# Optimization experiments

Hardware: AMD Instinct MI355X
Metric: run time of the kernel (lower is better)

The kernel has to match this reference:

```python
import jax, jax.numpy as jnp
import numpy as np

B, N, C = 16, 1024, 768
E, H, D, K = 8, 192, 4, 2


def setup_inputs() -> dict:
    key = jax.random.key(0)
    ks = jax.random.split(key, 8)
    std = 0.02
    return {
        "x": jax.random.normal(ks[0], (B, N, C), jnp.float32),
        "task_ids": jax.random.randint(ks[1], (B,), 0, D),
        "eps": jax.random.normal(ks[2], (B, N, E), jnp.float32),
        "gate_w": jax.random.normal(ks[3], (D, C, 2 * E), jnp.float32) * std,
        "fc1_w": jax.random.normal(ks[4], (E, H, C), jnp.float32) * std,
        "fc1_b": jnp.zeros((E, H), jnp.float32),
        "fc2_w": jax.random.normal(ks[5], (E, C, H), jnp.float32) * std,
        "fc2_b": jnp.zeros((E, C), jnp.float32),
    }


def reference(x, task_ids, eps, gate_w, fc1_w, fc1_b, fc2_w, fc2_b):
    # per-sample gate selected by domain/task id: [B,N,2E]
    total_w = jnp.einsum("bnc,bce->bne", x, gate_w[task_ids])
    clean_logits, raw_noise = jnp.split(total_w, 2, axis=-1)  # [B,N,E] each
    noise_stddev = jax.nn.softplus(raw_noise) + 0.01
    logits = clean_logits + eps * noise_stddev  # [B,N,E]
    exp_wise_sum = logits.sum(axis=1)  # [B,E]

    top_k_logits, top_k_idx = jax.lax.top_k(exp_wise_sum, K)  # [B,K]
    m1 = top_k_logits.min(axis=1, keepdims=True)
    m2 = top_k_logits.max(axis=1, keepdims=True)
    scaled = (top_k_logits - m1) / (m2 - m1 + 1e-6)
    top_k_gates = jax.nn.softmax(scaled, axis=1)  # [B,K]

    gates_full = jnp.zeros((B, E), x.dtype).at[
        jnp.arange(B)[:, None], top_k_idx
    ].set(top_k_gates)  # [B,E]

    # dense all-expert adapter compute (faithful to original torch.stack)
    h = jnp.einsum("bnc,ehc->benh", x, fc1_w) + fc1_b[None, :, None, :]
    h = jax.nn.gelu(h, approximate=False)
    expert_outs = jnp.einsum("benh,ech->benc", h, fc2_w) + fc2_b[None, :, None, :]

    tot_x = jnp.einsum("be,benc->bnc", gates_full, expert_outs)
    return x + tot_x
```

## Files before the change

kernel.cpp:

```cpp
#include <hip/hip_runtime.h>

#define B_ 16
#define N_ 1024
#define C_ 768
#define E_ 8
#define H_ 192

typedef __bf16 bf16x8 __attribute__((ext_vector_type(8)));
typedef float  f32x4  __attribute__((ext_vector_type(4)));

__global__ __launch_bounds__(256) void prep_kernel(
    const float* __restrict__ w1, const float* __restrict__ w2,
    const float* __restrict__ gw,
    __bf16* __restrict__ pw1, __bf16* __restrict__ pw2,
    float* __restrict__ gwT) {
  int idx = blockIdx.x * 256 + threadIdx.x;
  const int nW4 = (E_ * H_ * C_) / 4;
  if (idx >= nW4) return;
  int flat = idx * 4;
  int e = flat / (H_ * C_);
  int r = flat - e * (H_ * C_);

  {
    float4 a = *(const float4*)(w1 + (size_t)flat);
    int n = r / C_;
    int c = r - n * C_;
    size_t o = ((size_t)(e * 24 + (c >> 5)) * 192 + n) * 32 + (c & 31);
    pw1[o + 0] = (__bf16)a.x; pw1[o + 1] = (__bf16)a.y;
    pw1[o + 2] = (__bf16)a.z; pw1[o + 3] = (__bf16)a.w;
  }
  {
    float4 a = *(const float4*)(w2 + (size_t)flat);
    int n = r / H_;
    int h = r - n * H_;
    size_t o = ((size_t)(e * 6 + (h >> 5)) * 768 + n) * 32 + (h & 31);
    pw2[o + 0] = (__bf16)a.x; pw2[o + 1] = (__bf16)a.y;
    pw2[o + 2] = (__bf16)a.z; pw2[o + 3] = (__bf16)a.w;
  }
  if (idx < (4 * 16 * C_) / 4) {
    int f = idx * 4;
    int d = f / (16 * C_);
    int rr = f - d * (16 * C_);
    int j = rr / C_;
    int c = rr - j * C_;
    const float* src = gw + (size_t)d * C_ * 16 + j;
    float4 v;
    v.x = src[(size_t)(c + 0) * 16]; v.y = src[(size_t)(c + 1) * 16];
    v.z = src[(size_t)(c + 2) * 16]; v.w = src[(size_t)(c + 3) * 16];
    *(float4*)(gwT + (size_t)f) = v;
  }
}

__global__ __launch_bounds__(256, 3) void gate_kernel(
    const float* __restrict__ x, const int* __restrict__ task_ids,
    const float* __restrict__ eps, const float* __restrict__ gwT,
    float* __restrict__ psums) {
  const int b = blockIdx.x >> 6;
  const int token0 = (blockIdx.x & 63) * 16;
  const int tid = threadIdx.x;

  __shared__ __align__(16) float xt[16][772];
  __shared__ float sc[16][16];
  __shared__ float red[16][8];

  const float* xbase = x + ((size_t)b * N_ + token0) * C_;
  for (int it = 0; it < 12; ++it) {
    int chunk = it * 256 + tid;
    int row = chunk / 192;
    int col4 = chunk - row * 192;
    float4 v = *(const float4*)(xbase + (size_t)row * C_ + col4 * 4);
    *(float4*)&xt[row][col4 * 4] = v;
  }
  __syncthreads();

  const int t = tid & 15;
  const int j = tid >> 4;
  const int task = task_ids[b];
  const float* wrow = gwT + ((size_t)task * 16 + j) * C_;
  float acc = 0.0f;
#pragma unroll 4
  for (int c = 0; c < C_; c += 4) {
    float4 xv = *(const float4*)&xt[t][c];
    float4 wv = *(const float4*)(wrow + c);
    acc += xv.x * wv.x + xv.y * wv.y + xv.z * wv.z + xv.w * wv.w;
  }
  sc[t][j] = acc;
  __syncthreads();
  if (j < 8) {
    float clean = sc[t][j];
    float raw = sc[t][j + 8];
    float sp = (raw > 20.0f) ? raw : log1pf(expf(raw));
    red[t][j] = clean +
        eps[((size_t)b * N_ + token0 + t) * E_ + j] * (sp + 0.01f);
  }
  __syncthreads();
  if (tid < 8) {
    float s = 0.0f;
#pragma unroll
    for (int tt = 0; tt < 16; ++tt) s += red[tt][tid];
    psums[(size_t)blockIdx.x * 8 + tid] = s;
  }
}

#define SMEM_EXPERT (64 * 776 * 2 + 64 * 200 * 2 + 32)

__global__ __launch_bounds__(512, 2) void expert_kernel(
    const float* __restrict__ x, const __bf16* __restrict__ pw1,
    const __bf16* __restrict__ pw2, const float* __restrict__ fc1_b,
    const float* __restrict__ fc2_b, const float* __restrict__ psums,
    float* __restrict__ out) {
  const int bid = blockIdx.x;
  const int sxc = bid >> 3;
  const int b = (bid & 7) * 2 + (sxc >> 4);
  const int token0 = (sxc & 15) * 64;
  const int tid = threadIdx.x;
  const int wave = tid >> 6;
  const int wm = wave >> 2;
  const int wn = wave & 3;
  const int lane = tid & 63;
  const int ln = lane & 15;
  const int q8 = (lane >> 4) * 8;
  const int q4 = (lane >> 4) * 4;
  const int arow = wm * 32;

  extern __shared__ char smem[];
  __bf16 (*xs)[776] = reinterpret_cast<__bf16(*)[776]>(smem);
  __bf16 (*hs)[200] = reinterpret_cast<__bf16(*)[200]>(smem + 99328);
  float* smc = reinterpret_cast<float*>(smem + 99328 + 25600);

  {
    float v = psums[(((size_t)b << 6) | lane) * 8 + wave];
#pragma unroll
    for (int off = 32; off; off >>= 1) v += __shfl_down(v, off);
    if (lane == 0) smc[wave] = v;
  }
  __syncthreads();

  int e_idx[2]; float gate_v[2];
  {
    float best = -INFINITY, best2 = -INFINITY;
    int i1 = 0, i2 = 0;
#pragma unroll
    for (int e = 0; e < E_; ++e) {
      float v = smc[e];
      if (v > best) { best2 = best; i2 = i1; best = v; i1 = e; }
      else if (v > best2) { best2 = v; i2 = e; }
    }
    float d = best - best2;
    float st = d / (d + 1e-6f);
    float et = expf(st);
    e_idx[0] = i1; gate_v[0] = et / (et + 1.0f);
    e_idx[1] = i2; gate_v[1] = 1.0f / (et + 1.0f);
  }

  bf16x8 bq[4][3];
  {
    const __bf16* w1l = pw1 + (size_t)e_idx[0] * (24 * 192 * 32)
                            + (size_t)(wn * 48 + ln) * 32 + q8;
#pragma unroll
    for (int k0 = 0; k0 < 4; ++k0)
#pragma unroll
      for (int jj = 0; jj < 3; ++jj)
        bq[k0][jj] = *(const bf16x8*)(w1l + (size_t)k0 * 6144 + jj * 512);
  }

  const float* xbase = x + ((size_t)b * N_ + token0) * C_;
  for (int it = 0; it < 12; ++it) {
    int chunk = it * 512 + tid;
    int row = chunk / 96;
    int col8 = chunk - row * 96;
    const float* p = xbase + (size_t)row * C_ + col8 * 8;
    float4 v0 = *(const float4*)p;
    float4 v1 = *(const float4*)(p + 4);
    bf16x8 tv;
    tv[0] = (__bf16)v0.x; tv[1] = (__bf16)v0.y; tv[2] = (__bf16)v0.z; tv[3] = (__bf16)v0.w;
    tv[4] = (__bf16)v1.x; tv[5] = (__bf16)v1.y; tv[6] = (__bf16)v1.z; tv[7] = (__bf16)v1.w;
    *(bf16x8*)&xs[row][col8 * 8] = tv;
  }
  __syncthreads();

  f32x4 c2[2][12] = {};

  for (int kx = 0; kx < 2; ++kx) {
    const int e = e_idx[kx];
    const float g = gate_v[kx];

    const __bf16* w1l = pw1 + (size_t)e * (24 * 192 * 32)
                            + (size_t)(wn * 48 + ln) * 32 + q8;
    if (kx == 1) {
#pragma unroll
      for (int k0 = 0; k0 < 4; ++k0)
#pragma unroll
        for (int jj = 0; jj < 3; ++jj)
          bq[k0][jj] = *(const bf16x8*)(w1l + (size_t)k0 * 6144 + jj * 512);
    }
    bf16x8 aq[4][2];
#pragma unroll
    for (int k0 = 0; k0 < 4; ++k0) {
      aq[k0][0] = *(const bf16x8*)&xs[arow + ln][k0 * 32 + q8];
      aq[k0][1] = *(const bf16x8*)&xs[arow + 16 + ln][k0 * 32 + q8];
    }
    f32x4 c1[2][3] = {};
#pragma unroll
    for (int kb = 0; kb < 24; ++kb) {
      const int p = kb & 3;
#pragma unroll
      for (int jj = 0; jj < 3; ++jj) {
        c1[0][jj] = __builtin_amdgcn_mfma_f32_16x16x32_bf16(aq[p][0], bq[p][jj], c1[0][jj], 0, 0, 0);
        c1[1][jj] = __builtin_amdgcn_mfma_f32_16x16x32_bf16(aq[p][1], bq[p][jj], c1[1][jj], 0, 0, 0);
      }
      if (kb < 20) {
        const int kn = kb + 4;
        const __bf16* nx = w1l + (size_t)kn * 6144;
#pragma unroll
        for (int jj = 0; jj < 3; ++jj) bq[p][jj] = *(const bf16x8*)(nx + jj * 512);
        aq[p][0] = *(const bf16x8*)&xs[arow + ln][kn * 32 + q8];
        aq[p][1] = *(const bf16x8*)&xs[arow + 16 + ln][kn * 32 + q8];
      }
    }
#pragma unroll
    for (int jj = 0; jj < 3; ++jj) {
      int col = wn * 48 + jj * 16 + ln;
      float b1 = fc1_b[e * H_ + col];
#pragma unroll
      for (int m = 0; m < 2; ++m) {
#pragma unroll
        for (int r = 0; r < 4; ++r) {
          int row = arow + m * 16 + q4 + r;
          float v = c1[m][jj][r] + b1;
          float gl = 0.5f * v * (1.0f + erff(v * 0.70710678118f));
          hs[row][col] = (__bf16)(g * gl);
        }
      }
    }
    __syncthreads();

    const __bf16* w2l = pw2 + (size_t)e * (6 * 768 * 32)
                            + (size_t)(wn * 192 + ln) * 32 + q8;
    bf16x8 bh[3][6], av[3][2];
#pragma unroll
    for (int s0 = 0; s0 < 3; ++s0) {
      const __bf16* src = w2l + (size_t)(s0 >> 1) * 24576;
#pragma unroll
      for (int jj = 0; jj < 6; ++jj)
        bh[s0][jj] = *(const bf16x8*)(src + ((s0 & 1) * 6 + jj) * 512);
    }
    av[0][0] = *(const bf16x8*)&hs[arow + ln][q8];
    av[0][1] = *(const bf16x8*)&hs[arow + 16 + ln][q8];
    av[1][0] = *(const bf16x8*)&hs[arow + ln][32 + q8];
    av[1][1] = *(const bf16x8*)&hs[arow + 16 + ln][32 + q8];
#pragma unroll
    for (int st = 0; st < 12; ++st) {
      const int kb = st >> 1;
      const int half = st & 1;
      const int p = st % 3;
      const int as = kb % 3;
#pragma unroll
      for (int jj = 0; jj < 6; ++jj) {
        const int cj = half * 6 + jj;
        c2[0][cj] = __builtin_amdgcn_mfma_f32_16x16x32_bf16(av[as][0], bh[p][jj], c2[0][cj], 0, 0, 0);
        c2[1][cj] = __builtin_amdgcn_mfma_f32_16x16x32_bf16(av[as][1], bh[p][jj], c2[1][cj], 0, 0, 0);
      }
      if (st < 9) {
        const int s2 = st + 3;
        const int kb2 = s2 >> 1, half2 = s2 & 1;
        const __bf16* src = w2l + (size_t)kb2 * 24576;
#pragma unroll
        for (int jj = 0; jj < 6; ++jj)
          bh[p][jj] = *(const bf16x8*)(src + (half2 * 6 + jj) * 512);
        if (half2 == 0) {
          av[kb2 % 3][0] = *(const bf16x8*)&hs[arow + ln][kb2 * 32 + q8];
          av[kb2 % 3][1] = *(const bf16x8*)&hs[arow + 16 + ln][kb2 * 32 + q8];
        }
      }
    }
    __syncthreads();
  }

  const float* xr = x + ((size_t)b * N_ + token0) * C_;
  float* outr = out + ((size_t)b * N_ + token0) * C_;
#pragma unroll
  for (int jj = 0; jj < 12; ++jj) {
    int col = wn * 192 + jj * 16 + ln;
    float b2t = gate_v[0] * fc2_b[e_idx[0] * C_ + col] +
                gate_v[1] * fc2_b[e_idx[1] * C_ + col];
#pragma unroll
    for (int m = 0; m < 2; ++m) {
#pragma unroll
      for (int r = 0; r < 4; ++r) {
        int row = arow + m * 16 + q4 + r;
        size_t off = (size_t)row * C_ + col;
        outr[off] = xr[off] + c2[m][jj][r] + b2t;
      }
    }
  }
}

extern "C" void kernel_launch(void* const* d_in, const int* in_sizes, int n_in,
                              void* d_out, int out_size, void* d_ws, size_t ws_size,
                              hipStream_t stream) {
  const float* x      = (const float*)d_in[0];
  const int*   task   = (const int*)d_in[1];
  const float* eps    = (const float*)d_in[2];
  const float* gate_w = (const float*)d_in[3];
  const float* fc1_w  = (const float*)d_in[4];
  const float* fc1_b  = (const float*)d_in[5];
  const float* fc2_w  = (const float*)d_in[6];
  const float* fc2_b  = (const float*)d_in[7];
  float* out = (float*)d_out;

  const size_t nW = (size_t)E_ * H_ * C_;
  __bf16* pw1 = (__bf16*)d_ws;
  __bf16* pw2 = pw1 + nW;
  float* gwT   = (float*)((char*)d_ws + 2 * nW * sizeof(__bf16));
  float* psums = gwT + 4 * 16 * C_;

  prep_kernel<<<(nW / 4 + 255) / 256, 256, 0, stream>>>(fc1_w, fc2_w, gate_w,
                                                        pw1, pw2, gwT);
  gate_kernel<<<B_ * 64, 256, 0, stream>>>(x, task, eps, gwT, psums);

  hipFuncSetAttribute(reinterpret_cast<const void*>(expert_kernel),
                      hipFuncAttributeMaxDynamicSharedMemorySize, SMEM_EXPERT);
  expert_kernel<<<B_ * 16, 512, SMEM_EXPERT, stream>>>(
      x, pw1, pw2, fc1_b, fc2_b, psums, out);
}
```

Baseline: 206.0 us.

## Double expert kernel block to 1024 threads, one 16-row tile per wave

The expert kernel moves from 512 to 1024 threads per block, so each wave computes a 16-row M tile instead of 32 rows. The weight and activation prefetch pipelines become shallower (3-stage for fc1, double-buffered for fc2), which cuts per-thread registers to allow more waves. The trade-off is that each B-fragment weight load from global memory now feeds only one MFMA row tile, so weight traffic per FLOP doubles. With launch_bounds(1024,4), register pressure may also force spills.

Result: slower. 228.0 us (+10.7%).

```diff
diff --git a/kernel.cpp b/kernel.cpp
--- a/kernel.cpp
+++ b/kernel.cpp
@@ -104,7 +104,7 @@
 
 #define SMEM_EXPERT (64 * 776 * 2 + 64 * 200 * 2 + 32)
 
-__global__ __launch_bounds__(512, 2) void expert_kernel(
+__global__ __launch_bounds__(1024, 4) void expert_kernel(
     const float* __restrict__ x, const __bf16* __restrict__ pw1,
     const __bf16* __restrict__ pw2, const float* __restrict__ fc1_b,
     const float* __restrict__ fc2_b, const float* __restrict__ psums,
@@ -121,14 +121,14 @@
   const int ln = lane & 15;
   const int q8 = (lane >> 4) * 8;
   const int q4 = (lane >> 4) * 4;
-  const int arow = wm * 32;
+  const int arow = wm * 16;
 
   extern __shared__ char smem[];
   __bf16 (*xs)[776] = reinterpret_cast<__bf16(*)[776]>(smem);
   __bf16 (*hs)[200] = reinterpret_cast<__bf16(*)[200]>(smem + 99328);
   float* smc = reinterpret_cast<float*>(smem + 99328 + 25600);
 
-  {
+  if (wave < 8) {
     float v = psums[(((size_t)b << 6) | lane) * 8 + wave];
 #pragma unroll
     for (int off = 32; off; off >>= 1) v += __shfl_down(v, off);
@@ -153,20 +153,20 @@
     e_idx[1] = i2; gate_v[1] = 1.0f / (et + 1.0f);
   }
 
-  bf16x8 bq[4][3];
+  bf16x8 bq[3][3];
   {
     const __bf16* w1l = pw1 + (size_t)e_idx[0] * (24 * 192 * 32)
                             + (size_t)(wn * 48 + ln) * 32 + q8;
 #pragma unroll
-    for (int k0 = 0; k0 < 4; ++k0)
+    for (int k0 = 0; k0 < 3; ++k0)
 #pragma unroll
       for (int jj = 0; jj < 3; ++jj)
         bq[k0][jj] = *(const bf16x8*)(w1l + (size_t)k0 * 6144 + jj * 512);
   }
 
   const float* xbase = x + ((size_t)b * N_ + token0) * C_;
-  for (int it = 0; it < 12; ++it) {
-    int chunk = it * 512 + tid;
+  for (int it = 0; it < 6; ++it) {
+    int chunk = it * 1024 + tid;
     int row = chunk / 96;
     int col8 = chunk - row * 96;
     const float* p = xbase + (size_t)row * C_ + col8 * 8;
@@ -179,7 +179,7 @@
   }
   __syncthreads();
 
-  f32x4 c2[2][12] = {};
+  f32x4 c2[12] = {};
 
   for (int kx = 0; kx < 2; ++kx) {
     const int e = e_idx[kx];
@@ -189,33 +189,28 @@
                             + (size_t)(wn * 48 + ln) * 32 + q8;
     if (kx == 1) {
 #pragma unroll
-      for (int k0 = 0; k0 < 4; ++k0)
+      for (int k0 = 0; k0 < 3; ++k0)
 #pragma unroll
         for (int jj = 0; jj < 3; ++jj)
           bq[k0][jj] = *(const bf16x8*)(w1l + (size_t)k0 * 6144 + jj * 512);
     }
-    bf16x8 aq[4][2];
-#pragma unroll
-    for (int k0 = 0; k0 < 4; ++k0) {
-      aq[k0][0] = *(const bf16x8*)&xs[arow + ln][k0 * 32 + q8];
-      aq[k0][1] = *(const bf16x8*)&xs[arow + 16 + ln][k0 * 32 + q8];
-    }
-    f32x4 c1[2][3] = {};
+    bf16x8 aq[3];
+#pragma unroll
+    for (int k0 = 0; k0 < 3; ++k0)
+      aq[k0] = *(const bf16x8*)&xs[arow + ln][k0 * 32 + q8];
+    f32x4 c1[3] = {};
 #pragma unroll
     for (int kb = 0; kb < 24; ++kb) {
-      const int p = kb & 3;
-#pragma unroll
-      for (int jj = 0; jj < 3; ++jj) {
-        c1[0][jj] = __builtin_amdgcn_mfma_f32_16x16x32_bf16(aq[p][0], bq[p][jj], c1[0][jj], 0, 0, 0);
-        c1[1][jj] = __builtin_amdgcn_mfma_f32_16x16x32_bf16(aq[p][1], bq[p][jj], c1[1][jj], 0, 0, 0);
-      }
-      if (kb < 20) {
-        const int kn = kb + 4;
+      const int p = kb % 3;
+#pragma unroll
+      for (int jj = 0; jj < 3; ++jj)
+        c1[jj] = __builtin_amdgcn_mfma_f32_16x16x32_bf16(aq[p], bq[p][jj], c1[jj], 0, 0, 0);
+      if (kb < 21) {
+        const int kn = kb + 3;
         const __bf16* nx = w1l + (size_t)kn * 6144;
 #pragma unroll
         for (int jj = 0; jj < 3; ++jj) bq[p][jj] = *(const bf16x8*)(nx + jj * 512);
-        aq[p][0] = *(const bf16x8*)&xs[arow + ln][kn * 32 + q8];
-        aq[p][1] = *(const bf16x8*)&xs[arow + 16 + ln][kn * 32 + q8];
+        aq[p] = *(const bf16x8*)&xs[arow + ln][kn * 32 + q8];
       }
     }
 #pragma unroll
@@ -223,55 +218,40 @@
       int col = wn * 48 + jj * 16 + ln;
       float b1 = fc1_b[e * H_ + col];
 #pragma unroll
-      for (int m = 0; m < 2; ++m) {
-#pragma unroll
-        for (int r = 0; r < 4; ++r) {
-          int row = arow + m * 16 + q4 + r;
-          float v = c1[m][jj][r] + b1;
-          float gl = 0.5f * v * (1.0f + erff(v * 0.70710678118f));
-          hs[row][col] = (__bf16)(g * gl);
-        }
+      for (int r = 0; r < 4; ++r) {
+        int row = arow + q4 + r;
+        float v = c1[jj][r] + b1;
+        float gl = 0.5f * v * (1.0f + erff(v * 0.70710678118f));
+        hs[row][col] = (__bf16)(g * gl);
       }
     }
     __syncthreads();
 
     const __bf16* w2l = pw2 + (size_t)e * (6 * 768 * 32)
                             + (size_t)(wn * 192 + ln) * 32 + q8;
-    bf16x8 bh[3][6], av[3][2];
-#pragma unroll
-    for (int s0 = 0; s0 < 3; ++s0) {
-      const __bf16* src = w2l + (size_t)(s0 >> 1) * 24576;
-#pragma unroll
-      for (int jj = 0; jj < 6; ++jj)
-        bh[s0][jj] = *(const bf16x8*)(src + ((s0 & 1) * 6 + jj) * 512);
-    }
-    av[0][0] = *(const bf16x8*)&hs[arow + ln][q8];
-    av[0][1] = *(const bf16x8*)&hs[arow + 16 + ln][q8];
-    av[1][0] = *(const bf16x8*)&hs[arow + ln][32 + q8];
-    av[1][1] = *(const bf16x8*)&hs[arow + 16 + ln][32 + q8];
+    bf16x8 bh[2][6], av[2];
+#pragma unroll
+    for (int jj = 0; jj < 6; ++jj) bh[0][jj] = *(const bf16x8*)(w2l + jj * 512);
+    av[0] = *(const bf16x8*)&hs[arow + ln][q8];
 #pragma unroll
     for (int st = 0; st < 12; ++st) {
       const int kb = st >> 1;
       const int half = st & 1;
-      const int p = st % 3;
-      const int as = kb % 3;
+      const int p = st & 1;
+      if (st < 11) {
+        const int s2 = st + 1;
+        const int kb2 = s2 >> 1, half2 = s2 & 1;
+        const __bf16* src = w2l + (size_t)kb2 * 24576;
+#pragma unroll
+        for (int jj = 0; jj < 6; ++jj)
+          bh[p ^ 1][jj] = *(const bf16x8*)(src + (half2 * 6 + jj) * 512);
+        if (half2 == 0)
+          av[kb2 & 1] = *(const bf16x8*)&hs[arow + ln][kb2 * 32 + q8];
+      }
 #pragma unroll
       for (int jj = 0; jj < 6; ++jj) {
         const int cj = half * 6 + jj;
-        c2[0][cj] = __builtin_amdgcn_mfma_f32_16x16x32_bf16(av[as][0], bh[p][jj], c2[0][cj], 0, 0, 0);
-        c2[1][cj] = __builtin_amdgcn_mfma_f32_16x16x32_bf16(av[as][1], bh[p][jj], c2[1][cj], 0, 0, 0);
-      }
-      if (st < 9) {
-        const int s2 = st + 3;
-        const int kb2 = s2 >> 1, half2 = s2 & 1;
-        const __bf16* src = w2l + (size_t)kb2 * 24576;
-#pragma unroll
-        for (int jj = 0; jj < 6; ++jj)
-          bh[p][jj] = *(const bf16x8*)(src + (half2 * 6 + jj) * 512);
-        if (half2 == 0) {
-          av[kb2 % 3][0] = *(const bf16x8*)&hs[arow + ln][kb2 * 32 + q8];
-          av[kb2 % 3][1] = *(const bf16x8*)&hs[arow + 16 + ln][kb2 * 32 + q8];
-        }
+        c2[cj] = __builtin_amdgcn_mfma_f32_16x16x32_bf16(av[kb & 1], bh[p][jj], c2[cj], 0, 0, 0);
       }
     }
     __syncthreads();
@@ -285,13 +265,10 @@
     float b2t = gate_v[0] * fc2_b[e_idx[0] * C_ + col] +
                 gate_v[1] * fc2_b[e_idx[1] * C_ + col];
 #pragma unroll
-    for (int m = 0; m < 2; ++m) {
-#pragma unroll
-      for (int r = 0; r < 4; ++r) {
-        int row = arow + m * 16 + q4 + r;
-        size_t off = (size_t)row * C_ + col;
-        outr[off] = xr[off] + c2[m][jj][r] + b2t;
-      }
+    for (int r = 0; r < 4; ++r) {
+      int row = arow + q4 + r;
+      size_t off = (size_t)row * C_ + col;
+      outr[off] = xr[off] + c2[jj][r] + b2t;
     }
   }
 }
@@ -321,6 +298,6 @@
 
   hipFuncSetAttribute(reinterpret_cast<const void*>(expert_kernel),
                       hipFuncAttributeMaxDynamicSharedMemorySize, SMEM_EXPERT);
-  expert_kernel<<<B_ * 16, 512, SMEM_EXPERT, stream>>>(
+  expert_kernel<<<B_ * 16, 1024, SMEM_EXPERT, stream>>>(
       x, pw1, pw2, fc1_b, fc2_b, psums, out);
 }
```

## Use 12 waves per block with 6-way column split in expert kernel

Applied to the files above, without the earlier changes.

Raises the expert kernel block from 512 to 768 threads, so 12 waves are arranged as 2x6 instead of 2x4. Each wave now covers 32 hidden columns in the first GEMM and 128 output columns in the second. The second GEMM is restructured into two passes with double-buffered weight prefetch, which cuts per-wave register pressure and exposes more waves for latency hiding. The grid stays at 256 blocks, so each block gets more parallelism but loses some per-wave prefetch depth. Launch bounds become (768,3), which tightens the register cap and could cause spills.

Result: no change. 205.6 us (-0.2%).

```diff
diff --git a/kernel.cpp b/kernel.cpp
--- a/kernel.cpp
+++ b/kernel.cpp
@@ -104,7 +104,7 @@
 
 #define SMEM_EXPERT (64 * 776 * 2 + 64 * 200 * 2 + 32)
 
-__global__ __launch_bounds__(512, 2) void expert_kernel(
+__global__ __launch_bounds__(768, 3) void expert_kernel(
     const float* __restrict__ x, const __bf16* __restrict__ pw1,
     const __bf16* __restrict__ pw2, const float* __restrict__ fc1_b,
     const float* __restrict__ fc2_b, const float* __restrict__ psums,
@@ -115,8 +115,8 @@
   const int token0 = (sxc & 15) * 64;
   const int tid = threadIdx.x;
   const int wave = tid >> 6;
-  const int wm = wave >> 2;
-  const int wn = wave & 3;
+  const int wm = wave / 6;
+  const int wn = wave - wm * 6;
   const int lane = tid & 63;
   const int ln = lane & 15;
   const int q8 = (lane >> 4) * 8;
@@ -128,7 +128,7 @@
   __bf16 (*hs)[200] = reinterpret_cast<__bf16(*)[200]>(smem + 99328);
   float* smc = reinterpret_cast<float*>(smem + 99328 + 25600);
 
-  {
+  if (wave < 8) {
     float v = psums[(((size_t)b << 6) | lane) * 8 + wave];
 #pragma unroll
     for (int off = 32; off; off >>= 1) v += __shfl_down(v, off);
@@ -153,20 +153,20 @@
     e_idx[1] = i2; gate_v[1] = 1.0f / (et + 1.0f);
   }
 
-  bf16x8 bq[4][3];
+  bf16x8 bq[3][2];
   {
     const __bf16* w1l = pw1 + (size_t)e_idx[0] * (24 * 192 * 32)
-                            + (size_t)(wn * 48 + ln) * 32 + q8;
-#pragma unroll
-    for (int k0 = 0; k0 < 4; ++k0)
-#pragma unroll
-      for (int jj = 0; jj < 3; ++jj)
+                            + (size_t)(wn * 32 + ln) * 32 + q8;
+#pragma unroll
+    for (int k0 = 0; k0 < 3; ++k0)
+#pragma unroll
+      for (int jj = 0; jj < 2; ++jj)
         bq[k0][jj] = *(const bf16x8*)(w1l + (size_t)k0 * 6144 + jj * 512);
   }
 
   const float* xbase = x + ((size_t)b * N_ + token0) * C_;
-  for (int it = 0; it < 12; ++it) {
-    int chunk = it * 512 + tid;
+  for (int it = 0; it < 8; ++it) {
+    int chunk = it * 768 + tid;
     int row = chunk / 96;
     int col8 = chunk - row * 96;
     const float* p = xbase + (size_t)row * C_ + col8 * 8;
@@ -179,48 +179,48 @@
   }
   __syncthreads();
 
-  f32x4 c2[2][12] = {};
+  f32x4 c2[2][8] = {};
 
   for (int kx = 0; kx < 2; ++kx) {
     const int e = e_idx[kx];
     const float g = gate_v[kx];
 
     const __bf16* w1l = pw1 + (size_t)e * (24 * 192 * 32)
-                            + (size_t)(wn * 48 + ln) * 32 + q8;
+                            + (size_t)(wn * 32 + ln) * 32 + q8;
     if (kx == 1) {
 #pragma unroll
-      for (int k0 = 0; k0 < 4; ++k0)
-#pragma unroll
-        for (int jj = 0; jj < 3; ++jj)
+      for (int k0 = 0; k0 < 3; ++k0)
+#pragma unroll
+        for (int jj = 0; jj < 2; ++jj)
           bq[k0][jj] = *(const bf16x8*)(w1l + (size_t)k0 * 6144 + jj * 512);
     }
-    bf16x8 aq[4][2];
-#pragma unroll
-    for (int k0 = 0; k0 < 4; ++k0) {
+    bf16x8 aq[3][2];
+#pragma unroll
+    for (int k0 = 0; k0 < 3; ++k0) {
       aq[k0][0] = *(const bf16x8*)&xs[arow + ln][k0 * 32 + q8];
       aq[k0][1] = *(const bf16x8*)&xs[arow + 16 + ln][k0 * 32 + q8];
     }
-    f32x4 c1[2][3] = {};
+    f32x4 c1[2][2] = {};
 #pragma unroll
     for (int kb = 0; kb < 24; ++kb) {
-      const int p = kb & 3;
-#pragma unroll
-      for (int jj = 0; jj < 3; ++jj) {
+      const int p = kb % 3;
+#pragma unroll
+      for (int jj = 0; jj < 2; ++jj) {
         c1[0][jj] = __builtin_amdgcn_mfma_f32_16x16x32_bf16(aq[p][0], bq[p][jj], c1[0][jj], 0, 0, 0);
         c1[1][jj] = __builtin_amdgcn_mfma_f32_16x16x32_bf16(aq[p][1], bq[p][jj], c1[1][jj], 0, 0, 0);
       }
-      if (kb < 20) {
-        const int kn = kb + 4;
+      if (kb < 21) {
+        const int kn = kb + 3;
         const __bf16* nx = w1l + (size_t)kn * 6144;
 #pragma unroll
-        for (int jj = 0; jj < 3; ++jj) bq[p][jj] = *(const bf16x8*)(nx + jj * 512);
+        for (int jj = 0; jj < 2; ++jj) bq[p][jj] = *(const bf16x8*)(nx + jj * 512);
         aq[p][0] = *(const bf16x8*)&xs[arow + ln][kn * 32 + q8];
         aq[p][1] = *(const bf16x8*)&xs[arow + 16 + ln][kn * 32 + q8];
       }
     }
 #pragma unroll
-    for (int jj = 0; jj < 3; ++jj) {
-      int col = wn * 48 + jj * 16 + ln;
+    for (int jj = 0; jj < 2; ++jj) {
+      int col = wn * 32 + jj * 16 + ln;
       float b1 = fc1_b[e * H_ + col];
 #pragma unroll
       for (int m = 0; m < 2; ++m) {
@@ -235,42 +235,31 @@
     }
     __syncthreads();
 
-    const __bf16* w2l = pw2 + (size_t)e * (6 * 768 * 32)
-                            + (size_t)(wn * 192 + ln) * 32 + q8;
-    bf16x8 bh[3][6], av[3][2];
-#pragma unroll
-    for (int s0 = 0; s0 < 3; ++s0) {
-      const __bf16* src = w2l + (size_t)(s0 >> 1) * 24576;
-#pragma unroll
-      for (int jj = 0; jj < 6; ++jj)
-        bh[s0][jj] = *(const bf16x8*)(src + ((s0 & 1) * 6 + jj) * 512);
-    }
-    av[0][0] = *(const bf16x8*)&hs[arow + ln][q8];
-    av[0][1] = *(const bf16x8*)&hs[arow + 16 + ln][q8];
-    av[1][0] = *(const bf16x8*)&hs[arow + ln][32 + q8];
-    av[1][1] = *(const bf16x8*)&hs[arow + 16 + ln][32 + q8];
-#pragma unroll
-    for (int st = 0; st < 12; ++st) {
-      const int kb = st >> 1;
-      const int half = st & 1;
-      const int p = st % 3;
-      const int as = kb % 3;
-#pragma unroll
-      for (int jj = 0; jj < 6; ++jj) {
-        const int cj = half * 6 + jj;
-        c2[0][cj] = __builtin_amdgcn_mfma_f32_16x16x32_bf16(av[as][0], bh[p][jj], c2[0][cj], 0, 0, 0);
-        c2[1][cj] = __builtin_amdgcn_mfma_f32_16x16x32_bf16(av[as][1], bh[p][jj], c2[1][cj], 0, 0, 0);
-      }
-      if (st < 9) {
-        const int s2 = st + 3;
-        const int kb2 = s2 >> 1, half2 = s2 & 1;
-        const __bf16* src = w2l + (size_t)kb2 * 24576;
-#pragma unroll
-        for (int jj = 0; jj < 6; ++jj)
-          bh[p][jj] = *(const bf16x8*)(src + (half2 * 6 + jj) * 512);
-        if (half2 == 0) {
-          av[kb2 % 3][0] = *(const bf16x8*)&hs[arow + ln][kb2 * 32 + q8];
-          av[kb2 % 3][1] = *(const bf16x8*)&hs[arow + 16 + ln][kb2 * 32 + q8];
+#pragma unroll
+    for (int pass = 0; pass < 2; ++pass) {
+      const __bf16* w2l = pw2 + (size_t)e * (6 * 768 * 32)
+                              + (size_t)(wn * 128 + pass * 64 + ln) * 32 + q8;
+      bf16x8 bh[2][4], av[2][2];
+#pragma unroll
+      for (int jj = 0; jj < 4; ++jj) bh[0][jj] = *(const bf16x8*)(w2l + jj * 512);
+      av[0][0] = *(const bf16x8*)&hs[arow + ln][q8];
+      av[0][1] = *(const bf16x8*)&hs[arow + 16 + ln][q8];
+#pragma unroll
+      for (int kb = 0; kb < 6; ++kb) {
+        const int p = kb & 1;
+        if (kb < 5) {
+          const __bf16* src = w2l + (size_t)(kb + 1) * 24576;
+#pragma unroll
+          for (int jj = 0; jj < 4; ++jj)
+            bh[p ^ 1][jj] = *(const bf16x8*)(src + jj * 512);
+          av[p ^ 1][0] = *(const bf16x8*)&hs[arow + ln][(kb + 1) * 32 + q8];
+          av[p ^ 1][1] = *(const bf16x8*)&hs[arow + 16 + ln][(kb + 1) * 32 + q8];
+        }
+#pragma unroll
+        for (int jj = 0; jj < 4; ++jj) {
+          const int cj = pass * 4 + jj;
+          c2[0][cj] = __builtin_amdgcn_mfma_f32_16x16x32_bf16(av[p][0], bh[p][jj], c2[0][cj], 0, 0, 0);
+          c2[1][cj] = __builtin_amdgcn_mfma_f32_16x16x32_bf16(av[p][1], bh[p][jj], c2[1][cj], 0, 0, 0);
         }
       }
     }
@@ -280,8 +269,8 @@
   const float* xr = x + ((size_t)b * N_ + token0) * C_;
   float* outr = out + ((size_t)b * N_ + token0) * C_;
 #pragma unroll
-  for (int jj = 0; jj < 12; ++jj) {
-    int col = wn * 192 + jj * 16 + ln;
+  for (int jj = 0; jj < 8; ++jj) {
+    int col = wn * 128 + jj * 16 + ln;
     float b2t = gate_v[0] * fc2_b[e_idx[0] * C_ + col] +
                 gate_v[1] * fc2_b[e_idx[1] * C_ + col];
 #pragma unroll
@@ -321,6 +310,6 @@
 
   hipFuncSetAttribute(reinterpret_cast<const void*>(expert_kernel),
                       hipFuncAttributeMaxDynamicSharedMemorySize, SMEM_EXPERT);
-  expert_kernel<<<B_ * 16, 512, SMEM_EXPERT, stream>>>(
+  expert_kernel<<<B_ * 16, 768, SMEM_EXPERT, stream>>>(
       x, pw1, pw2, fc1_b, fc2_b, psums, out);
 }
```

## Stage expert weights through shared-memory triple buffer with swizzled layout

Applied to the files above, without the earlier changes.

Replaces per-wave direct global loads of fc1/fc2 weight fragments with a block-cooperative pipeline. Each 12KB weight tile is fetched once into registers, written into a triple-buffered, XOR-swizzled LDS staging area, and read back as MFMA fragments. The aim is to stop the weight reads that were duplicated across the two wm wave rows and to overlap the global fetch with compute. The cost is a __syncthreads per tile (96 per block), extra LDS traffic, and more shared memory, which may limit how many blocks fit per CU.

Result: slower. 429.3 us (+108.4%).

```diff
diff --git a/kernel.cpp b/kernel.cpp
--- a/kernel.cpp
+++ b/kernel.cpp
@@ -102,7 +102,11 @@
   }
 }
 
-#define SMEM_EXPERT (64 * 776 * 2 + 64 * 200 * 2 + 32)
+#define XS_OFF   0
+#define HS_OFF   99328
+#define STG_OFF  (99328 + 25600)
+#define SMC_OFF  (STG_OFF + 36864)
+#define SMEM_EXPERT (SMC_OFF + 32)
 
 __global__ __launch_bounds__(512, 2) void expert_kernel(
     const float* __restrict__ x, const __bf16* __restrict__ pw1,
@@ -119,14 +123,16 @@
   const int wn = wave & 3;
   const int lane = tid & 63;
   const int ln = lane & 15;
-  const int q8 = (lane >> 4) * 8;
-  const int q4 = (lane >> 4) * 4;
+  const int qq = lane >> 4;
+  const int q8 = qq * 8;
+  const int q4 = qq * 4;
   const int arow = wm * 32;
 
   extern __shared__ char smem[];
-  __bf16 (*xs)[776] = reinterpret_cast<__bf16(*)[776]>(smem);
-  __bf16 (*hs)[200] = reinterpret_cast<__bf16(*)[200]>(smem + 99328);
-  float* smc = reinterpret_cast<float*>(smem + 99328 + 25600);
+  __bf16 (*xs)[776] = reinterpret_cast<__bf16(*)[776]>(smem + XS_OFF);
+  __bf16 (*hs)[200] = reinterpret_cast<__bf16(*)[200]>(smem + HS_OFF);
+  char* stg = smem + STG_OFF;
+  float* smc = reinterpret_cast<float*>(smem + SMC_OFF);
 
   {
     float v = psums[(((size_t)b << 6) | lane) * 8 + wave];
@@ -153,16 +159,55 @@
     e_idx[1] = i2; gate_v[1] = 1.0f / (et + 1.0f);
   }
 
-  bf16x8 bq[4][3];
-  {
-    const __bf16* w1l = pw1 + (size_t)e_idx[0] * (24 * 192 * 32)
-                            + (size_t)(wn * 48 + ln) * 32 + q8;
-#pragma unroll
-    for (int k0 = 0; k0 < 4; ++k0)
-#pragma unroll
-      for (int jj = 0; jj < 3; ++jj)
-        bq[k0][jj] = *(const bf16x8*)(w1l + (size_t)k0 * 6144 + jj * 512);
-  }
+  const char* wsrc[2][2];
+  wsrc[0][0] = (const char*)(pw1 + (size_t)e_idx[0] * 147456);
+  wsrc[0][1] = (const char*)(pw2 + (size_t)e_idx[0] * 147456);
+  wsrc[1][0] = (const char*)(pw1 + (size_t)e_idx[1] * 147456);
+  wsrc[1][1] = (const char*)(pw2 + (size_t)e_idx[1] * 147456);
+
+#define TSRC(s) \
+  (((s) % 48) < 24 \
+     ? wsrc[(s) / 48][0] + (size_t)((s) % 48) * 12288 \
+     : wsrc[(s) / 48][1] + (size_t)(((s) % 48 - 24) % 6) * 49152 \
+                         + (size_t)(((s) % 48 - 24) / 6) * 12288)
+
+#define ISSUE(s, d0, d1)                                          \
+  if ((s) < 96) {                                                 \
+    const char* gsrc_ = TSRC(s);                                  \
+    d0 = *(const uint4*)(gsrc_ + (size_t)tid * 16);               \
+    if (tid < 256) d1 = *(const uint4*)(gsrc_ + 8192 + (size_t)tid * 16); \
+  }
+
+#define WCHUNK(bufp, c, d)                                        \
+  {                                                               \
+    int r_ = (c) >> 2, p_ = (c) & 3, sw_ = r_ & 7;                \
+    char* rp_ = (bufp) + r_ * 64;                                 \
+    *(uint2*)(rp_ + (((p_ << 1)    ) ^ sw_) * 8) = make_uint2((d).x, (d).y); \
+    *(uint2*)(rp_ + (((p_ << 1) | 1) ^ sw_) * 8) = make_uint2((d).z, (d).w); \
+  }
+#define WTILE(s, d0, d1)                                          \
+  if ((s) < 96) {                                                 \
+    char* buf_ = stg + ((s) % 3) * 12288;                         \
+    WCHUNK(buf_, tid, d0);                                        \
+    if (tid < 256) WCHUNK(buf_, 512 + tid, d1);                   \
+  }
+
+#define RFRAG(dst, bufp, n)                                       \
+  {                                                               \
+    const char* rp_ = (bufp) + (n) * 64;                          \
+    int sw_ = (n) & 7;                                            \
+    uint2 lo_ = *(const uint2*)(rp_ + (((qq << 1)    ) ^ sw_) * 8); \
+    uint2 hi_ = *(const uint2*)(rp_ + (((qq << 1) | 1) ^ sw_) * 8); \
+    union { uint v[4]; bf16x8 f; } u_;                            \
+    u_.v[0] = lo_.x; u_.v[1] = lo_.y; u_.v[2] = hi_.x; u_.v[3] = hi_.y; \
+    dst = u_.f;                                                   \
+  }
+
+  uint4 rg0[3], rg1[3];
+
+  ISSUE(0, rg0[0], rg1[0]);
+  ISSUE(1, rg0[1], rg1[1]);
+  ISSUE(2, rg0[2], rg1[2]);
 
   const float* xbase = x + ((size_t)b * N_ + token0) * C_;
   for (int it = 0; it < 12; ++it) {
@@ -177,111 +222,74 @@
     tv[4] = (__bf16)v1.x; tv[5] = (__bf16)v1.y; tv[6] = (__bf16)v1.z; tv[7] = (__bf16)v1.w;
     *(bf16x8*)&xs[row][col8 * 8] = tv;
   }
+  WTILE(0, rg0[0], rg1[0]);
   __syncthreads();
 
   f32x4 c2[2][12] = {};
 
-  for (int kx = 0; kx < 2; ++kx) {
-    const int e = e_idx[kx];
-    const float g = gate_v[kx];
-
-    const __bf16* w1l = pw1 + (size_t)e * (24 * 192 * 32)
-                            + (size_t)(wn * 48 + ln) * 32 + q8;
-    if (kx == 1) {
-#pragma unroll
-      for (int k0 = 0; k0 < 4; ++k0)
-#pragma unroll
-        for (int jj = 0; jj < 3; ++jj)
-          bq[k0][jj] = *(const bf16x8*)(w1l + (size_t)k0 * 6144 + jj * 512);
-    }
-    bf16x8 aq[4][2];
-#pragma unroll
-    for (int k0 = 0; k0 < 4; ++k0) {
-      aq[k0][0] = *(const bf16x8*)&xs[arow + ln][k0 * 32 + q8];
-      aq[k0][1] = *(const bf16x8*)&xs[arow + 16 + ln][k0 * 32 + q8];
-    }
+#pragma unroll
+  for (int ex = 0; ex < 2; ++ex) {
+    const int e = e_idx[ex];
+    const float g = gate_v[ex];
     f32x4 c1[2][3] = {};
-#pragma unroll
-    for (int kb = 0; kb < 24; ++kb) {
-      const int p = kb & 3;
-#pragma unroll
-      for (int jj = 0; jj < 3; ++jj) {
-        c1[0][jj] = __builtin_amdgcn_mfma_f32_16x16x32_bf16(aq[p][0], bq[p][jj], c1[0][jj], 0, 0, 0);
-        c1[1][jj] = __builtin_amdgcn_mfma_f32_16x16x32_bf16(aq[p][1], bq[p][jj], c1[1][jj], 0, 0, 0);
-      }
-      if (kb < 20) {
-        const int kn = kb + 4;
-        const __bf16* nx = w1l + (size_t)kn * 6144;
-#pragma unroll
-        for (int jj = 0; jj < 3; ++jj) bq[p][jj] = *(const bf16x8*)(nx + jj * 512);
-        aq[p][0] = *(const bf16x8*)&xs[arow + ln][kn * 32 + q8];
-        aq[p][1] = *(const bf16x8*)&xs[arow + 16 + ln][kn * 32 + q8];
-      }
-    }
-#pragma unroll
-    for (int jj = 0; jj < 3; ++jj) {
-      int col = wn * 48 + jj * 16 + ln;
-      float b1 = fc1_b[e * H_ + col];
-#pragma unroll
-      for (int m = 0; m < 2; ++m) {
-#pragma unroll
-        for (int r = 0; r < 4; ++r) {
-          int row = arow + m * 16 + q4 + r;
-          float v = c1[m][jj][r] + b1;
-          float gl = 0.5f * v * (1.0f + erff(v * 0.70710678118f));
-          hs[row][col] = (__bf16)(g * gl);
+
+#pragma unroll
+    for (int t = 0; t < 48; ++t) {
+      const int s = ex * 48 + t;
+      ISSUE(s + 3, rg0[s % 3], rg1[s % 3]);
+      WTILE(s + 1, rg0[(s + 1) % 3], rg1[(s + 1) % 3]);
+      __syncthreads();
+
+      const char* buf = stg + (s % 3) * 12288;
+      if (t < 24) {
+        bf16x8 a0 = *(const bf16x8*)&xs[arow + ln][t * 32 + q8];
+        bf16x8 a1 = *(const bf16x8*)&xs[arow + 16 + ln][t * 32 + q8];
+#pragma unroll
+        for (int j = 0; j < 3; ++j) {
+          bf16x8 bf;
+          RFRAG(bf, buf, wn * 48 + j * 16 + ln);
+          c1[0][j] = __builtin_amdgcn_mfma_f32_16x16x32_bf16(a0, bf, c1[0][j], 0, 0, 0);
+          c1[1][j] = __builtin_amdgcn_mfma_f32_16x16x32_bf16(a1, bf, c1[1][j], 0, 0, 0);
+        }
+        if (t == 23) {
+#pragma unroll
+          for (int j = 0; j < 3; ++j) {
+            int col = wn * 48 + j * 16 + ln;
+            float b1 = fc1_b[e * H_ + col];
+#pragma unroll
+            for (int m = 0; m < 2; ++m) {
+#pragma unroll
+              for (int r = 0; r < 4; ++r) {
+                int row = arow + m * 16 + q4 + r;
+                float v = c1[m][j][r] + b1;
+                float gl = 0.5f * v * (1.0f + erff(v * 0.70710678118f));
+                hs[row][col] = (__bf16)(g * gl);
+              }
+            }
+          }
+        }
+      } else {
+        const int slice = (t - 24) / 6;
+        const int kb = (t - 24) % 6;
+        bf16x8 a0 = *(const bf16x8*)&hs[arow + ln][kb * 32 + q8];
+        bf16x8 a1 = *(const bf16x8*)&hs[arow + 16 + ln][kb * 32 + q8];
+#pragma unroll
+        for (int j = 0; j < 3; ++j) {
+          bf16x8 bf;
+          RFRAG(bf, buf, wn * 48 + j * 16 + ln);
+          const int cj = slice * 3 + j;
+          c2[0][cj] = __builtin_amdgcn_mfma_f32_16x16x32_bf16(a0, bf, c2[0][cj], 0, 0, 0);
+          c2[1][cj] = __builtin_amdgcn_mfma_f32_16x16x32_bf16(a1, bf, c2[1][cj], 0, 0, 0);
         }
       }
     }
-    __syncthreads();
-
-    const __bf16* w2l = pw2 + (size_t)e * (6 * 768 * 32)
-                            + (size_t)(wn * 192 + ln) * 32 + q8;
-    bf16x8 bh[3][6], av[3][2];
-#pragma unroll
-    for (int s0 = 0; s0 < 3; ++s0) {
-      const __bf16* src = w2l + (size_t)(s0 >> 1) * 24576;
-#pragma unroll
-      for (int jj = 0; jj < 6; ++jj)
-        bh[s0][jj] = *(const bf16x8*)(src + ((s0 & 1) * 6 + jj) * 512);
-    }
-    av[0][0] = *(const bf16x8*)&hs[arow + ln][q8];
-    av[0][1] = *(const bf16x8*)&hs[arow + 16 + ln][q8];
-    av[1][0] = *(const bf16x8*)&hs[arow + ln][32 + q8];
-    av[1][1] = *(const bf16x8*)&hs[arow + 16 + ln][32 + q8];
-#pragma unroll
-    for (int st = 0; st < 12; ++st) {
-      const int kb = st >> 1;
-      const int half = st & 1;
-      const int p = st % 3;
-      const int as = kb % 3;
-#pragma unroll
-      for (int jj = 0; jj < 6; ++jj) {
-        const int cj = half * 6 + jj;
-        c2[0][cj] = __builtin_amdgcn_mfma_f32_16x16x32_bf16(av[as][0], bh[p][jj], c2[0][cj], 0, 0, 0);
-        c2[1][cj] = __builtin_amdgcn_mfma_f32_16x16x32_bf16(av[as][1], bh[p][jj], c2[1][cj], 0, 0, 0);
-      }
-      if (st < 9) {
-        const int s2 = st + 3;
-        const int kb2 = s2 >> 1, half2 = s2 & 1;
-        const __bf16* src = w2l + (size_t)kb2 * 24576;
-#pragma unroll
-        for (int jj = 0; jj < 6; ++jj)
-          bh[p][jj] = *(const bf16x8*)(src + (half2 * 6 + jj) * 512);
-        if (half2 == 0) {
-          av[kb2 % 3][0] = *(const bf16x8*)&hs[arow + ln][kb2 * 32 + q8];
-          av[kb2 % 3][1] = *(const bf16x8*)&hs[arow + 16 + ln][kb2 * 32 + q8];
-        }
-      }
-    }
-    __syncthreads();
   }
 
   const float* xr = x + ((size_t)b * N_ + token0) * C_;
   float* outr = out + ((size_t)b * N_ + token0) * C_;
 #pragma unroll
   for (int jj = 0; jj < 12; ++jj) {
-    int col = wn * 192 + jj * 16 + ln;
+    int col = (jj / 3) * 192 + wn * 48 + (jj % 3) * 16 + ln;
     float b2t = gate_v[0] * fc2_b[e_idx[0] * C_ + col] +
                 gate_v[1] * fc2_b[e_idx[1] * C_ + col];
 #pragma unroll
```
